# Kernel optimization log

Hardware: AMD Instinct MI355X
Metric: run time of the kernel (lower is better)

## Reference

```python
import jax, jax.numpy as jnp
import numpy as np

NUM_HEADS = 16
WINDOW = 256
DIM = 1024


def setup_inputs() -> dict:
    key = jax.random.key(0)
    k1, k2, k3, k4, k5 = jax.random.split(key, 5)
    B, L, D = 2, 2048, DIM
    s = 1.0 / np.sqrt(D)
    return {
        "x": jax.random.normal(k1, (B, L, D), dtype=jnp.float32),
        "in_proj_w": jax.random.uniform(k2, (3 * D, D), dtype=jnp.float32, minval=-s, maxval=s),
        "in_proj_b": jax.random.uniform(k3, (3 * D,), dtype=jnp.float32, minval=-s, maxval=s),
        "out_w": jax.random.uniform(k4, (D, D), dtype=jnp.float32, minval=-s, maxval=s),
        "out_b": jax.random.uniform(k5, (D,), dtype=jnp.float32, minval=-s, maxval=s),
    }


def reference(x, in_proj_w, in_proj_b, out_w, out_b):
    B, L, D = x.shape
    H = NUM_HEADS
    hd = D // H

    # combined qkv projection, as in nn.MultiheadAttention
    qkv = x @ in_proj_w.T + in_proj_b          # [B, L, 3D]
    q, k, v = jnp.split(qkv, 3, axis=-1)
    q = q.reshape(B, L, H, hd).transpose(0, 2, 1, 3)  # [B, H, L, hd]
    k = k.reshape(B, L, H, hd).transpose(0, 2, 1, 3)
    v = v.reshape(B, L, H, hd).transpose(0, 2, 1, 3)

    scale = 1.0 / jnp.sqrt(jnp.asarray(hd, dtype=x.dtype))
    scores = jnp.einsum("bhqd,bhkd->bhqk", q * scale, k)  # [B, H, L, L]

    # sliding-window causal mask: allowed iff i-window < j <= i
    i = jnp.arange(L)[:, None]
    j = jnp.arange(L)[None, :]
    allowed = (j <= i) & (j > i - WINDOW)                  # [L, L]
    scores = jnp.where(allowed[None, None], scores, -jnp.inf)

    attn = jax.nn.softmax(scores, axis=-1)
    out = jnp.einsum("bhqk,bhkd->bhqd", attn, v)           # [B, H, L, hd]
    out = out.transpose(0, 2, 1, 3).reshape(B, L, D)
    return out @ out_w.T + out_b
```

## Files before the change

kernel.cpp:

```cpp
#include <hip/hip_runtime.h>


#define SEQ_L 2048
#define WIN   256

typedef __bf16 bf16x8 __attribute__((ext_vector_type(8)));
typedef float  f32x4  __attribute__((ext_vector_type(4)));

template<int X> struct ic { static constexpr int v = X; };

__device__ __forceinline__ unsigned short f32_to_bf16(float f) {
  unsigned int u = __float_as_uint(f);
  u += 0x7FFFu + ((u >> 16) & 1u);
  return (unsigned short)(u >> 16);
}

__device__ __forceinline__ void async16(const unsigned short* g, unsigned short* l) {
  __builtin_amdgcn_global_load_lds(
      (const __attribute__((address_space(1))) unsigned int*)g,
      (__attribute__((address_space(3))) unsigned int*)l, 16, 0, 0);
}

__global__ void cast_all(const float* __restrict__ x,  unsigned short* __restrict__ xo,
                         const float* __restrict__ w1, unsigned short* __restrict__ w1o,
                         const float* __restrict__ w2, unsigned short* __restrict__ w2o) {
  int i = blockIdx.x * 256 + threadIdx.x;
  const float* in; unsigned short* out; int k;
  if (i < 1048576)       { in = x;  out = xo;  k = i; }
  else if (i < 1835008)  { in = w1; out = w1o; k = i - 1048576; }
  else                   { in = w2; out = w2o; k = i - 1835008; }
  float4 v = ((const float4*)in)[k];
  ushort4 o;
  o.x = f32_to_bf16(v.x); o.y = f32_to_bf16(v.y);
  o.z = f32_to_bf16(v.z); o.w = f32_to_bf16(v.w);
  ((ushort4*)out)[k] = o;
}

__global__ __launch_bounds__(512, 2) void gemm_qkv(
    const unsigned short* __restrict__ A,
    const unsigned short* __restrict__ Bt,
    const float* __restrict__ bias,
    unsigned short* __restrict__ C, int M, int N, int K)
{
  __shared__ unsigned short As[2][256 * 64];
  __shared__ unsigned short Bs[2][192 * 64];

  const int tid  = threadIdx.x;
  const int lane = tid & 63;
  const int w    = tid >> 6;
  const int wr   = w >> 2;
  const int wc   = w & 3;
  const int quad = lane >> 4;
  const int l16  = lane & 15;
  const int lrow = (lane >> 3) & 7;
  const int scol = (lane & 7) ^ lrow;

  const long m0 = (long)blockIdx.y * 256;
  const long n0 = (long)blockIdx.x * 192;

  f32x4 acc[8][3];
#pragma unroll
  for (int i = 0; i < 8; ++i)
#pragma unroll
    for (int j = 0; j < 3; ++j)
#pragma unroll
      for (int r = 0; r < 4; ++r) acc[i][j][r] = 0.0f;

  auto stA = [&](int buf, int c, int kc) {
    async16(A + (m0 + c * 64 + w * 8 + lrow) * (long)K + kc + scol * 8,
            &As[buf][(c * 64 + w * 8) * 64]);
  };
  auto stB = [&](int buf, int c, int kc) {
    async16(Bt + (n0 + c * 64 + w * 8 + lrow) * (long)K + kc + scol * 8,
            &Bs[buf][(c * 64 + w * 8) * 64]);
  };
  auto hA0 = [&](int buf, int kc) { stA(buf, 0, kc); stA(buf, 2, kc); };
  auto hA1 = [&](int buf, int kc) { stA(buf, 1, kc); stA(buf, 3, kc); };
  auto hB  = [&](int buf, int kc) { stB(buf, 0, kc); stB(buf, 1, kc); stB(buf, 2, kc); };

  auto rdA = [&](bf16x8 (&af)[4], int buf, int QM, int kh) {
#pragma unroll
    for (int mi = 0; mi < 4; ++mi) {
      int rr = wr * 128 + QM * 64 + mi * 16 + l16;
      af[mi] = *(const bf16x8*)&As[buf][rr * 64 + (((kh * 4 + quad) ^ (rr & 7)) << 3)];
    }
  };
  auto rdB = [&](bf16x8 (&bq)[3], int buf, int kh) {
#pragma unroll
    for (int ni = 0; ni < 3; ++ni) {
      int rb = wc * 48 + ni * 16 + l16;
      bq[ni] = *(const bf16x8*)&Bs[buf][rb * 64 + (((kh * 4 + quad) ^ (rb & 7)) << 3)];
    }
  };
  auto cluster = [&](bf16x8 (&af)[4], bf16x8 (&bq)[3], int mb) {
    __builtin_amdgcn_s_setprio(1);
#pragma unroll
    for (int mi = 0; mi < 4; ++mi)
#pragma unroll
      for (int ni = 0; ni < 3; ++ni)
        acc[mb + mi][ni] = __builtin_amdgcn_mfma_f32_16x16x32_bf16(
            bq[ni], af[mi], acc[mb + mi][ni], 0, 0, 0);
    __builtin_amdgcn_s_setprio(0);
  };
  auto lgkm0 = [] {
    asm volatile("s_waitcnt lgkmcnt(0)" ::: "memory");
    __builtin_amdgcn_sched_barrier(0);
  };
  auto vmw = [](auto n) {
    constexpr int V = decltype(n)::v;
    if constexpr (V == 7)      asm volatile("s_waitcnt vmcnt(7)" ::: "memory");
    else if constexpr (V == 2) asm volatile("s_waitcnt vmcnt(2)" ::: "memory");
    else if constexpr (V == 0) asm volatile("s_waitcnt vmcnt(0)" ::: "memory");
  };

  hA0(0, 0); hB(0, 0); hA1(0, 0); hA0(1, 64); hB(1, 64);
  asm volatile("s_waitcnt vmcnt(7)" ::: "memory");
  __builtin_amdgcn_s_barrier();

  auto tile = [&](int T, auto s1, auto s4, auto v1, auto v4) {
    const int buf = T & 1;
    bf16x8 af[4], bq0[3], bq1[3];
    rdA(af, buf, 0, 0);
    rdB(bq0, buf, 0);
    if constexpr (decltype(s1)::v) hA1(buf ^ 1, (T + 1) * 64);
    lgkm0();
    cluster(af, bq0, 0);
    vmw(v1);
    __builtin_amdgcn_s_barrier();
    rdA(af, buf, 1, 0);
    lgkm0();
    cluster(af, bq0, 4);
    rdA(af, buf, 0, 1);
    rdB(bq1, buf, 1);
    lgkm0();
    cluster(af, bq1, 0);
    __builtin_amdgcn_s_barrier();
    rdA(af, buf, 1, 1);
    if constexpr (decltype(s4)::v) { hA0(buf, (T + 2) * 64); hB(buf, (T + 2) * 64); }
    lgkm0();
    cluster(af, bq1, 4);
    vmw(v4);
    __builtin_amdgcn_s_barrier();
  };

  const int NT = K >> 6;
#pragma unroll 1
  for (int T = 0; T < NT - 2; ++T) tile(T, ic<1>{}, ic<1>{}, ic<7>{}, ic<7>{});
  tile(NT - 2, ic<1>{}, ic<0>{}, ic<7>{}, ic<2>{});
  tile(NT - 1, ic<0>{}, ic<0>{}, ic<0>{}, ic<-1>{});

#pragma unroll
  for (int ni = 0; ni < 3; ++ni) {
    const int nb = wc * 48 + ni * 16 + quad * 4;
    const float4 bv = *(const float4*)&bias[n0 + nb];
#pragma unroll
    for (int qm = 0; qm < 2; ++qm)
#pragma unroll
      for (int mi = 0; mi < 4; ++mi) {
        long m = m0 + wr * 128 + qm * 64 + mi * 16 + l16;
        f32x4 a = acc[qm * 4 + mi][ni];
        ushort4 o;
        o.x = f32_to_bf16(a[0] + bv.x);
        o.y = f32_to_bf16(a[1] + bv.y);
        o.z = f32_to_bf16(a[2] + bv.z);
        o.w = f32_to_bf16(a[3] + bv.w);
        *(ushort4*)&C[m * (long)N + n0 + nb] = o;
      }
  }
}

template<int TBM, int TBN, int MI, int NI, int OUTBF>
__global__ __launch_bounds__(256) void gemm_nt(
    const unsigned short* __restrict__ A,
    const unsigned short* __restrict__ Bt,
    const float* __restrict__ bias,
    void* __restrict__ Cout, int M, int N, int K)
{
  __shared__ unsigned short As[TBM * 64];
  __shared__ unsigned short Bs[TBN * 64];

  const int tid  = threadIdx.x;
  const int lane = tid & 63;
  const int wave = tid >> 6;
  const int wr   = (wave >> 1) * (MI * 16);
  const int wc   = (wave & 1) * (NI * 16);
  const int quad = lane >> 4;
  const int l16  = lane & 15;
  const int lrow = lane >> 3;
  const int scol = (lane & 7) ^ lrow;

  const long m0 = (long)blockIdx.y * TBM;
  const long n0 = (long)blockIdx.x * TBN;

  f32x4 acc[MI][NI];
#pragma unroll
  for (int i = 0; i < MI; ++i)
#pragma unroll
    for (int j = 0; j < NI; ++j)
#pragma unroll
      for (int r = 0; r < 4; ++r) acc[i][j][r] = 0.0f;

  for (int k0 = 0; k0 < K; k0 += 64) {
#pragma unroll
    for (int p = 0; p < TBM / 32; ++p) {
      int rb = wave * (TBM / 4) + p * 8;
      async16(A + (m0 + rb + lrow) * (long)K + k0 + scol * 8, &As[rb * 64]);
    }
#pragma unroll
    for (int p = 0; p < TBN / 32; ++p) {
      int rb = wave * (TBN / 4) + p * 8;
      async16(Bt + (n0 + rb + lrow) * (long)K + k0 + scol * 8, &Bs[rb * 64]);
    }
    __syncthreads();
#pragma unroll
    for (int ks = 0; ks < 2; ++ks) {
      bf16x8 af[MI], bfv[NI];
#pragma unroll
      for (int mi = 0; mi < MI; ++mi) {
        int r = wr + mi * 16 + l16;
        af[mi] = *(const bf16x8*)(&As[r * 64 + ((ks * 4 + quad) ^ (r & 7)) * 8]);
      }
#pragma unroll
      for (int ni = 0; ni < NI; ++ni) {
        int r = wc + ni * 16 + l16;
        bfv[ni] = *(const bf16x8*)(&Bs[r * 64 + ((ks * 4 + quad) ^ (r & 7)) * 8]);
      }
#pragma unroll
      for (int mi = 0; mi < MI; ++mi)
#pragma unroll
        for (int ni = 0; ni < NI; ++ni)
          acc[mi][ni] = __builtin_amdgcn_mfma_f32_16x16x32_bf16(af[mi], bfv[ni], acc[mi][ni], 0, 0, 0);
    }
    __syncthreads();
  }

#pragma unroll
  for (int ni = 0; ni < NI; ++ni) {
    long col = n0 + wc + ni * 16 + l16;
    float bv = bias[col];
#pragma unroll
    for (int mi = 0; mi < MI; ++mi) {
      long rowb = m0 + wr + mi * 16 + quad * 4;
#pragma unroll
      for (int r = 0; r < 4; ++r) {
        float v = acc[mi][ni][r] + bv;
        if (OUTBF) ((unsigned short*)Cout)[(rowb + r) * N + col] = f32_to_bf16(v);
        else       ((float*)Cout)[(rowb + r) * N + col] = v;
      }
    }
  }
}

__global__ __launch_bounds__(256) void attn_kernel(
    const unsigned short* __restrict__ qkv,
    unsigned short* __restrict__ aout)
{
  __shared__ unsigned short Ks[64 * 72];
  __shared__ unsigned short Vt[64 * 72];
  __shared__ unsigned short Ps[4 * 16 * 72];

  const int tid  = threadIdx.x;
  const int w    = tid >> 6;
  const int lane = tid & 63;
  const int quad = lane >> 4;
  const int l16  = lane & 15;

  const int blk = blockIdx.x;
  const int qb  = blk & 15;
  const int h   = (blk >> 4) & 15;
  const int b   = blk >> 8;

  const int  i0 = qb * 128;
  const long rowbase = (long)b * SEQ_L;

  bf16x8 aq[2][2];
#pragma unroll
  for (int sub = 0; sub < 2; ++sub) {
    const unsigned short* qp =
        qkv + (rowbase + i0 + sub * 64 + w * 16 + l16) * 3072 + h * 64 + quad * 8;
    aq[sub][0] = *(const bf16x8*)(qp);
    aq[sub][1] = *(const bf16x8*)(qp + 32);
  }

  f32x4 o[2][4];
  float l_i[2][4];
#pragma unroll
  for (int sub = 0; sub < 2; ++sub)
#pragma unroll
    for (int ni = 0; ni < 4; ++ni)
#pragma unroll
      for (int r = 0; r < 4; ++r) { o[sub][ni][r] = 0.0f; l_i[sub][r] = 0.0f; }

  unsigned short* psw = &Ps[w * 16 * 72];

  const int j_begin = (i0 >= WIN) ? i0 - WIN : 0;

  for (int j0 = j_begin; j0 < i0 + 128; j0 += 64) {
    __syncthreads();
#pragma unroll
    for (int p = 0; p < 2; ++p) {
      int c = p * 256 + tid, row = c >> 3, col8 = c & 7;
      const unsigned short* base = qkv + (rowbase + j0 + row) * 3072 + h * 64 + col8 * 8;
      *(uint4*)(&Ks[row * 72 + col8 * 8]) = *(const uint4*)(base + 1024);
      unsigned short tmp[8];
      *(uint4*)tmp = *(const uint4*)(base + 2048);
      int rsw = row ^ (col8 << 3);
#pragma unroll
      for (int e = 0; e < 8; ++e)
        Vt[(col8 * 8 + e) * 72 + rsw] = tmp[e];
    }
    __syncthreads();

    bf16x8 kf[4][2];
#pragma unroll
    for (int g = 0; g < 4; ++g) {
      kf[g][0] = *(const bf16x8*)(&Ks[(g * 16 + l16) * 72 + quad * 8]);
      kf[g][1] = *(const bf16x8*)(&Ks[(g * 16 + l16) * 72 + 32 + quad * 8]);
    }
    bf16x8 vf[2][4];
#pragma unroll
    for (int kk = 0; kk < 2; ++kk)
#pragma unroll
      for (int ni = 0; ni < 4; ++ni) {
        int d  = ni * 16 + l16;
        int rb = (kk * 32 + quad * 8) ^ (((d >> 3) & 7) << 3);
        vf[kk][ni] = *(const bf16x8*)(&Vt[d * 72 + rb]);
      }

#pragma unroll
    for (int sub = 0; sub < 2; ++sub) {
      const int i0s = i0 + sub * 64 + w * 16;
      if (j0 > i0s + 15) continue;
      if (j0 + 63 + WIN <= i0s) continue;

      f32x4 s[4];
#pragma unroll
      for (int g = 0; g < 4; ++g) {
        f32x4 z;
#pragma unroll
        for (int r = 0; r < 4; ++r) z[r] = 0.0f;
        z = __builtin_amdgcn_mfma_f32_16x16x32_bf16(aq[sub][0], kf[g][0], z, 0, 0, 0);
        z = __builtin_amdgcn_mfma_f32_16x16x32_bf16(aq[sub][1], kf[g][1], z, 0, 0, 0);
        s[g] = z;
      }
#pragma unroll
      for (int g = 0; g < 4; ++g) {
        int j = j0 + g * 16 + l16;
#pragma unroll
        for (int r = 0; r < 4; ++r) {
          int i = i0s + quad * 4 + r;
          bool ok = (j <= i) && (j > i - WIN);
          float e = ok ? __expf(s[g][r] * 0.125f) : 0.0f;
          psw[(quad * 4 + r) * 72 + g * 16 + l16] = f32_to_bf16(e);
          l_i[sub][r] += e;
        }
      }
      asm volatile("s_waitcnt lgkmcnt(0)" ::: "memory");
#pragma unroll
      for (int kk = 0; kk < 2; ++kk) {
        bf16x8 ap = *(const bf16x8*)(&psw[l16 * 72 + kk * 32 + quad * 8]);
#pragma unroll
        for (int ni = 0; ni < 4; ++ni)
          o[sub][ni] = __builtin_amdgcn_mfma_f32_16x16x32_bf16(ap, vf[kk][ni], o[sub][ni], 0, 0, 0);
      }
    }
  }

#pragma unroll
  for (int sub = 0; sub < 2; ++sub)
#pragma unroll
    for (int r = 0; r < 4; ++r) {
      float rs = l_i[sub][r];
      rs += __shfl_xor(rs, 1);
      rs += __shfl_xor(rs, 2);
      rs += __shfl_xor(rs, 4);
      rs += __shfl_xor(rs, 8);
      float inv_l = 1.0f / rs;
      long row = rowbase + i0 + sub * 64 + w * 16 + quad * 4 + r;
#pragma unroll
      for (int ni = 0; ni < 4; ++ni)
        aout[row * 1024 + h * 64 + ni * 16 + l16] = f32_to_bf16(o[sub][ni][r] * inv_l);
    }
}

extern "C" void kernel_launch(void* const* d_in, const int* in_sizes, int n_in,
                              void* d_out, int out_size, void* d_ws, size_t ws_size,
                              hipStream_t stream)
{
  const float* x  = (const float*)d_in[0];
  const float* w1 = (const float*)d_in[1];
  const float* b1 = (const float*)d_in[2];
  const float* w2 = (const float*)d_in[3];
  const float* b2 = (const float*)d_in[4];
  float* out = (float*)d_out;

  char* ws = (char*)d_ws;
  unsigned short* x_bf   = (unsigned short*)(ws);
  unsigned short* w1_bf  = (unsigned short*)(ws + 8388608);
  unsigned short* w2_bf  = (unsigned short*)(ws + 14680064);
  unsigned short* qkv_bf = (unsigned short*)(ws + 16777216);
  unsigned short* at_bf  = (unsigned short*)(ws + 41943040);

  cast_all<<<8192, 256, 0, stream>>>(x, x_bf, w1, w1_bf, w2, w2_bf);

  dim3 g1(3072 / 192, 4096 / 256);
  gemm_qkv<<<g1, 512, 0, stream>>>(x_bf, w1_bf, b1, qkv_bf, 4096, 3072, 1024);

  attn_kernel<<<512, 256, 0, stream>>>(qkv_bf, at_bf);

  dim3 g2(1024 / 64, 4096 / 64);
  gemm_nt<64, 64, 2, 2, 0><<<g2, 256, 0, stream>>>(at_bf, w2_bf, b2, out, 4096, 1024, 1024);
}
```

Measured before the change: 155.0 us.

## Replace output projection GEMM with double-buffered 128x128 pipelined kernel

```diff
diff --git a/kernel.cpp b/kernel.cpp
--- a/kernel.cpp
+++ b/kernel.cpp
@@ -169,84 +169,120 @@
   }
 }
 
-template<int TBM, int TBN, int MI, int NI, int OUTBF>
-__global__ __launch_bounds__(256) void gemm_nt(
+__global__ __launch_bounds__(512, 4) void gemm_opj(
     const unsigned short* __restrict__ A,
     const unsigned short* __restrict__ Bt,
     const float* __restrict__ bias,
-    void* __restrict__ Cout, int M, int N, int K)
+    float* __restrict__ C, int M, int N, int K)
 {
-  __shared__ unsigned short As[TBM * 64];
-  __shared__ unsigned short Bs[TBN * 64];
+  __shared__ unsigned short As[2][128 * 64];
+  __shared__ unsigned short Bs[2][128 * 64];
 
   const int tid  = threadIdx.x;
   const int lane = tid & 63;
-  const int wave = tid >> 6;
-  const int wr   = (wave >> 1) * (MI * 16);
-  const int wc   = (wave & 1) * (NI * 16);
+  const int w    = tid >> 6;
+  const int wr   = w >> 2;
+  const int wc   = w & 3;
   const int quad = lane >> 4;
   const int l16  = lane & 15;
-  const int lrow = lane >> 3;
+  const int lrow = (lane >> 3) & 7;
   const int scol = (lane & 7) ^ lrow;
 
-  const long m0 = (long)blockIdx.y * TBM;
-  const long n0 = (long)blockIdx.x * TBN;
-
-  f32x4 acc[MI][NI];
-#pragma unroll
-  for (int i = 0; i < MI; ++i)
-#pragma unroll
-    for (int j = 0; j < NI; ++j)
+  const long m0 = (long)blockIdx.y * 128;
+  const long n0 = (long)blockIdx.x * 128;
+
+  f32x4 acc[4][2];
+#pragma unroll
+  for (int i = 0; i < 4; ++i)
+#pragma unroll
+    for (int j = 0; j < 2; ++j)
 #pragma unroll
       for (int r = 0; r < 4; ++r) acc[i][j][r] = 0.0f;
 
-  for (int k0 = 0; k0 < K; k0 += 64) {
-#pragma unroll
-    for (int p = 0; p < TBM / 32; ++p) {
-      int rb = wave * (TBM / 4) + p * 8;
-      async16(A + (m0 + rb + lrow) * (long)K + k0 + scol * 8, &As[rb * 64]);
-    }
-#pragma unroll
-    for (int p = 0; p < TBN / 32; ++p) {
-      int rb = wave * (TBN / 4) + p * 8;
-      async16(Bt + (n0 + rb + lrow) * (long)K + k0 + scol * 8, &Bs[rb * 64]);
-    }
-    __syncthreads();
-#pragma unroll
-    for (int ks = 0; ks < 2; ++ks) {
-      bf16x8 af[MI], bfv[NI];
-#pragma unroll
-      for (int mi = 0; mi < MI; ++mi) {
-        int r = wr + mi * 16 + l16;
-        af[mi] = *(const bf16x8*)(&As[r * 64 + ((ks * 4 + quad) ^ (r & 7)) * 8]);
-      }
-#pragma unroll
-      for (int ni = 0; ni < NI; ++ni) {
-        int r = wc + ni * 16 + l16;
-        bfv[ni] = *(const bf16x8*)(&Bs[r * 64 + ((ks * 4 + quad) ^ (r & 7)) * 8]);
-      }
-#pragma unroll
-      for (int mi = 0; mi < MI; ++mi)
-#pragma unroll
-        for (int ni = 0; ni < NI; ++ni)
-          acc[mi][ni] = __builtin_amdgcn_mfma_f32_16x16x32_bf16(af[mi], bfv[ni], acc[mi][ni], 0, 0, 0);
-    }
-    __syncthreads();
-  }
-
-#pragma unroll
-  for (int ni = 0; ni < NI; ++ni) {
-    long col = n0 + wc + ni * 16 + l16;
-    float bv = bias[col];
-#pragma unroll
-    for (int mi = 0; mi < MI; ++mi) {
-      long rowb = m0 + wr + mi * 16 + quad * 4;
-#pragma unroll
-      for (int r = 0; r < 4; ++r) {
-        float v = acc[mi][ni][r] + bv;
-        if (OUTBF) ((unsigned short*)Cout)[(rowb + r) * N + col] = f32_to_bf16(v);
-        else       ((float*)Cout)[(rowb + r) * N + col] = v;
-      }
+  auto stage = [&](int buf, int kc) {
+#pragma unroll
+    for (int c = 0; c < 2; ++c)
+      async16(A + (m0 + c * 64 + w * 8 + lrow) * (long)K + kc + scol * 8,
+              &As[buf][(c * 64 + w * 8) * 64]);
+#pragma unroll
+    for (int c = 0; c < 2; ++c)
+      async16(Bt + (n0 + c * 64 + w * 8 + lrow) * (long)K + kc + scol * 8,
+              &Bs[buf][(c * 64 + w * 8) * 64]);
+  };
+
+  auto rdA = [&](bf16x8 (&af)[4], int buf, int kh) {
+#pragma unroll
+    for (int mi = 0; mi < 4; ++mi) {
+      int rr = wr * 64 + mi * 16 + l16;
+      af[mi] = *(const bf16x8*)&As[buf][rr * 64 + (((kh * 4 + quad) ^ (rr & 7)) << 3)];
+    }
+  };
+  auto rdB = [&](bf16x8 (&bq)[2], int buf, int kh) {
+#pragma unroll
+    for (int ni = 0; ni < 2; ++ni) {
+      int rb = wc * 32 + ni * 16 + l16;
+      bq[ni] = *(const bf16x8*)&Bs[buf][rb * 64 + (((kh * 4 + quad) ^ (rb & 7)) << 3)];
+    }
+  };
+  auto cluster = [&](bf16x8 (&af)[4], bf16x8 (&bq)[2]) {
+    __builtin_amdgcn_s_setprio(1);
+#pragma unroll
+    for (int mi = 0; mi < 4; ++mi)
+#pragma unroll
+      for (int ni = 0; ni < 2; ++ni)
+        acc[mi][ni] = __builtin_amdgcn_mfma_f32_16x16x32_bf16(
+            bq[ni], af[mi], acc[mi][ni], 0, 0, 0);
+    __builtin_amdgcn_s_setprio(0);
+  };
+  auto lgkm0 = [] {
+    asm volatile("s_waitcnt lgkmcnt(0)" ::: "memory");
+    __builtin_amdgcn_sched_barrier(0);
+  };
+
+  stage(0, 0); stage(1, 64);
+  asm volatile("s_waitcnt vmcnt(4)" ::: "memory");
+  __builtin_amdgcn_s_barrier();
+
+  auto tile = [&](int T, auto s, auto v) {
+    const int buf = T & 1;
+    bf16x8 af[4], bq[2];
+    rdA(af, buf, 0);
+    rdB(bq, buf, 0);
+    lgkm0();
+    cluster(af, bq);
+    rdA(af, buf, 1);
+    rdB(bq, buf, 1);
+    lgkm0();
+    __builtin_amdgcn_s_barrier();
+    if constexpr (decltype(s)::v) stage(buf, (T + 2) * 64);
+    cluster(af, bq);
+    if constexpr (decltype(v)::v == 4)
+      asm volatile("s_waitcnt vmcnt(4)" ::: "memory");
+    else if constexpr (decltype(v)::v == 0)
+      asm volatile("s_waitcnt vmcnt(0)" ::: "memory");
+    __builtin_amdgcn_s_barrier();
+  };
+
+  const int NT = K >> 6;
+#pragma unroll 1
+  for (int T = 0; T < NT - 2; ++T) tile(T, ic<1>{}, ic<4>{});
+  tile(NT - 2, ic<0>{}, ic<0>{});
+  tile(NT - 1, ic<0>{}, ic<-1>{});
+
+#pragma unroll
+  for (int ni = 0; ni < 2; ++ni) {
+    const int nb = wc * 32 + ni * 16 + quad * 4;
+    const float4 bv = *(const float4*)&bias[n0 + nb];
+#pragma unroll
+    for (int mi = 0; mi < 4; ++mi) {
+      long m = m0 + wr * 64 + mi * 16 + l16;
+      f32x4 a = acc[mi][ni];
+      float4 o;
+      o.x = a[0] + bv.x;
+      o.y = a[1] + bv.y;
+      o.z = a[2] + bv.z;
+      o.w = a[3] + bv.w;
+      *(float4*)&C[m * (long)N + n0 + nb] = o;
     }
   }
 }
@@ -408,6 +444,6 @@
 
   attn_kernel<<<512, 256, 0, stream>>>(qkv_bf, at_bf);
 
-  dim3 g2(1024 / 64, 4096 / 64);
-  gemm_nt<64, 64, 2, 2, 0><<<g2, 256, 0, stream>>>(at_bf, w2_bf, b2, out, 4096, 1024, 1024);
-}
+  dim3 g2(1024 / 128, 4096 / 128);
+  gemm_opj<<<g2, 512, 0, stream>>>(at_bf, w2_bf, b2, out, 4096, 1024, 1024);
+}
```

Result: no change. 156.7 us (+1.1%).

## Prefetch all LDS fragments per tile and use partial lgkmcnt waits

Applied to the files above, without the earlier changes.

```diff
diff --git a/kernel.cpp b/kernel.cpp
--- a/kernel.cpp
+++ b/kernel.cpp
@@ -102,8 +102,11 @@
             bq[ni], af[mi], acc[mb + mi][ni], 0, 0, 0);
     __builtin_amdgcn_s_setprio(0);
   };
-  auto lgkm0 = [] {
-    asm volatile("s_waitcnt lgkmcnt(0)" ::: "memory");
+  auto lgkm = [](auto n) {
+    constexpr int V = decltype(n)::v;
+    if constexpr (V == 8)      asm volatile("s_waitcnt lgkmcnt(8)" ::: "memory");
+    else if constexpr (V == 4) asm volatile("s_waitcnt lgkmcnt(4)" ::: "memory");
+    else                       asm volatile("s_waitcnt lgkmcnt(0)" ::: "memory");
     __builtin_amdgcn_sched_barrier(0);
   };
   auto vmw = [](auto n) {
@@ -117,29 +120,28 @@
   asm volatile("s_waitcnt vmcnt(7)" ::: "memory");
   __builtin_amdgcn_s_barrier();
 
-  auto tile = [&](int T, auto s1, auto s4, auto v1, auto v4) {
+  auto tile = [&](int T, auto s1, auto s4, auto vS, auto vE) {
     const int buf = T & 1;
-    bf16x8 af[4], bq0[3], bq1[3];
-    rdA(af, buf, 0, 0);
-    rdB(bq0, buf, 0);
+    bf16x8 af00[4], af10[4], af01[4], af11[4], bq0[3], bq1[3];
+    rdA(af00, buf, 0, 0);
+    rdB(bq0,  buf, 0);
+    rdA(af01, buf, 0, 1);
+    rdB(bq1,  buf, 1);
     if constexpr (decltype(s1)::v) hA1(buf ^ 1, (T + 1) * 64);
-    lgkm0();
-    cluster(af, bq0, 0);
-    vmw(v1);
+    vmw(vS);
     __builtin_amdgcn_s_barrier();
-    rdA(af, buf, 1, 0);
-    lgkm0();
-    cluster(af, bq0, 4);
-    rdA(af, buf, 0, 1);
-    rdB(bq1, buf, 1);
-    lgkm0();
-    cluster(af, bq1, 0);
+    rdA(af10, buf, 1, 0);
+    rdA(af11, buf, 1, 1);
+    lgkm(ic<8>{});
+    cluster(af00, bq0, 0);
+    lgkm(ic<4>{});
+    cluster(af10, bq0, 4);
+    cluster(af01, bq1, 0);
+    lgkm(ic<0>{});
     __builtin_amdgcn_s_barrier();
-    rdA(af, buf, 1, 1);
     if constexpr (decltype(s4)::v) { hA0(buf, (T + 2) * 64); hB(buf, (T + 2) * 64); }
-    lgkm0();
-    cluster(af, bq1, 4);
-    vmw(v4);
+    cluster(af11, bq1, 4);
+    if constexpr (decltype(vE)::v >= 0) vmw(vE);
     __builtin_amdgcn_s_barrier();
   };
 
```

New measurement: 157.5 us. No clear change (+1.6%).

## Fuse activation fp32-to-bf16 cast into QKV GEMM A-tile loading

Applied to the files above, without the earlier changes.

```diff
diff --git a/kernel.cpp b/kernel.cpp
--- a/kernel.cpp
+++ b/kernel.cpp
@@ -21,14 +21,12 @@
       (__attribute__((address_space(3))) unsigned int*)l, 16, 0, 0);
 }
 
-__global__ void cast_all(const float* __restrict__ x,  unsigned short* __restrict__ xo,
-                         const float* __restrict__ w1, unsigned short* __restrict__ w1o,
-                         const float* __restrict__ w2, unsigned short* __restrict__ w2o) {
+__global__ void cast_w(const float* __restrict__ w1, unsigned short* __restrict__ w1o,
+                       const float* __restrict__ w2, unsigned short* __restrict__ w2o) {
   int i = blockIdx.x * 256 + threadIdx.x;
   const float* in; unsigned short* out; int k;
-  if (i < 1048576)       { in = x;  out = xo;  k = i; }
-  else if (i < 1835008)  { in = w1; out = w1o; k = i - 1048576; }
-  else                   { in = w2; out = w2o; k = i - 1835008; }
+  if (i < 786432) { in = w1; out = w1o; k = i; }
+  else            { in = w2; out = w2o; k = i - 786432; }
   float4 v = ((const float4*)in)[k];
   ushort4 o;
   o.x = f32_to_bf16(v.x); o.y = f32_to_bf16(v.y);
@@ -37,7 +35,7 @@
 }
 
 __global__ __launch_bounds__(512, 2) void gemm_qkv(
-    const unsigned short* __restrict__ A,
+    const float* __restrict__ X,
     const unsigned short* __restrict__ Bt,
     const float* __restrict__ bias,
     unsigned short* __restrict__ C, int M, int N, int K)
@@ -53,7 +51,8 @@
   const int quad = lane >> 4;
   const int l16  = lane & 15;
   const int lrow = (lane >> 3) & 7;
-  const int scol = (lane & 7) ^ lrow;
+  const int lcol = lane & 7;
+  const int scol = lcol ^ lrow;
 
   const long m0 = (long)blockIdx.y * 256;
   const long n0 = (long)blockIdx.x * 192;
@@ -66,17 +65,32 @@
 #pragma unroll
       for (int r = 0; r < 4; ++r) acc[i][j][r] = 0.0f;
 
-  auto stA = [&](int buf, int c, int kc) {
-    async16(A + (m0 + c * 64 + w * 8 + lrow) * (long)K + kc + scol * 8,
-            &As[buf][(c * 64 + w * 8) * 64]);
-  };
+  float4 rA[8];
+  auto loadA = [&](int kc) {
+#pragma unroll
+    for (int c = 0; c < 4; ++c) {
+      const float* src = X + (m0 + c * 64 + w * 8 + lrow) * (long)K + kc + lcol * 8;
+      rA[c * 2]     = *(const float4*)(src);
+      rA[c * 2 + 1] = *(const float4*)(src + 4);
+    }
+  };
+  auto writeA = [&](int buf) {
+#pragma unroll
+    for (int c = 0; c < 4; ++c) {
+      unsigned short tmp[8];
+      tmp[0] = f32_to_bf16(rA[c * 2].x);     tmp[1] = f32_to_bf16(rA[c * 2].y);
+      tmp[2] = f32_to_bf16(rA[c * 2].z);     tmp[3] = f32_to_bf16(rA[c * 2].w);
+      tmp[4] = f32_to_bf16(rA[c * 2 + 1].x); tmp[5] = f32_to_bf16(rA[c * 2 + 1].y);
+      tmp[6] = f32_to_bf16(rA[c * 2 + 1].z); tmp[7] = f32_to_bf16(rA[c * 2 + 1].w);
+      *(uint4*)&As[buf][(c * 64 + w * 8 + lrow) * 64 + (lcol ^ lrow) * 8] = *(uint4*)tmp;
+    }
+  };
+
   auto stB = [&](int buf, int c, int kc) {
     async16(Bt + (n0 + c * 64 + w * 8 + lrow) * (long)K + kc + scol * 8,
             &Bs[buf][(c * 64 + w * 8) * 64]);
   };
-  auto hA0 = [&](int buf, int kc) { stA(buf, 0, kc); stA(buf, 2, kc); };
-  auto hA1 = [&](int buf, int kc) { stA(buf, 1, kc); stA(buf, 3, kc); };
-  auto hB  = [&](int buf, int kc) { stB(buf, 0, kc); stB(buf, 1, kc); stB(buf, 2, kc); };
+  auto hB = [&](int buf, int kc) { stB(buf, 0, kc); stB(buf, 1, kc); stB(buf, 2, kc); };
 
   auto rdA = [&](bf16x8 (&af)[4], int buf, int QM, int kh) {
 #pragma unroll
@@ -106,48 +120,47 @@
     asm volatile("s_waitcnt lgkmcnt(0)" ::: "memory");
     __builtin_amdgcn_sched_barrier(0);
   };
-  auto vmw = [](auto n) {
-    constexpr int V = decltype(n)::v;
-    if constexpr (V == 7)      asm volatile("s_waitcnt vmcnt(7)" ::: "memory");
-    else if constexpr (V == 2) asm volatile("s_waitcnt vmcnt(2)" ::: "memory");
-    else if constexpr (V == 0) asm volatile("s_waitcnt vmcnt(0)" ::: "memory");
-  };
-
-  hA0(0, 0); hB(0, 0); hA1(0, 0); hA0(1, 64); hB(1, 64);
-  asm volatile("s_waitcnt vmcnt(7)" ::: "memory");
+
+  hB(0, 0);
+  loadA(0);
+  hB(1, 64);
+  asm volatile("s_waitcnt vmcnt(3)" ::: "memory");
+  writeA(0);
+  lgkm0();
   __builtin_amdgcn_s_barrier();
 
-  auto tile = [&](int T, auto s1, auto s4, auto v1, auto v4) {
+  auto tile = [&](int T, auto sA, auto sB) {
     const int buf = T & 1;
     bf16x8 af[4], bq0[3], bq1[3];
     rdA(af, buf, 0, 0);
     rdB(bq0, buf, 0);
-    if constexpr (decltype(s1)::v) hA1(buf ^ 1, (T + 1) * 64);
+    if constexpr (decltype(sA)::v) loadA((T + 1) * 64);
     lgkm0();
     cluster(af, bq0, 0);
-    vmw(v1);
-    __builtin_amdgcn_s_barrier();
     rdA(af, buf, 1, 0);
     lgkm0();
-    cluster(af, bq0, 4);
+    cluster(af, bq0, 2 * 2);
     rdA(af, buf, 0, 1);
     rdB(bq1, buf, 1);
     lgkm0();
     cluster(af, bq1, 0);
     __builtin_amdgcn_s_barrier();
     rdA(af, buf, 1, 1);
-    if constexpr (decltype(s4)::v) { hA0(buf, (T + 2) * 64); hB(buf, (T + 2) * 64); }
+    if constexpr (decltype(sA)::v) {
+      asm volatile("s_waitcnt vmcnt(0)" ::: "memory");
+      writeA(buf ^ 1);
+    }
+    if constexpr (decltype(sB)::v) hB(buf, (T + 2) * 64);
     lgkm0();
     cluster(af, bq1, 4);
-    vmw(v4);
     __builtin_amdgcn_s_barrier();
   };
 
   const int NT = K >> 6;
 #pragma unroll 1
-  for (int T = 0; T < NT - 2; ++T) tile(T, ic<1>{}, ic<1>{}, ic<7>{}, ic<7>{});
-  tile(NT - 2, ic<1>{}, ic<0>{}, ic<7>{}, ic<2>{});
-  tile(NT - 1, ic<0>{}, ic<0>{}, ic<0>{}, ic<-1>{});
+  for (int T = 0; T < NT - 2; ++T) tile(T, ic<1>{}, ic<1>{});
+  tile(NT - 2, ic<1>{}, ic<0>{});
+  tile(NT - 1, ic<0>{}, ic<0>{});
 
 #pragma unroll
   for (int ni = 0; ni < 3; ++ni) {
@@ -395,16 +408,15 @@
   float* out = (float*)d_out;
 
   char* ws = (char*)d_ws;
-  unsigned short* x_bf   = (unsigned short*)(ws);
   unsigned short* w1_bf  = (unsigned short*)(ws + 8388608);
   unsigned short* w2_bf  = (unsigned short*)(ws + 14680064);
   unsigned short* qkv_bf = (unsigned short*)(ws + 16777216);
   unsigned short* at_bf  = (unsigned short*)(ws + 41943040);
 
-  cast_all<<<8192, 256, 0, stream>>>(x, x_bf, w1, w1_bf, w2, w2_bf);
+  cast_w<<<4096, 256, 0, stream>>>(w1, w1_bf, w2, w2_bf);
 
   dim3 g1(3072 / 192, 4096 / 256);
-  gemm_qkv<<<g1, 512, 0, stream>>>(x_bf, w1_bf, b1, qkv_bf, 4096, 3072, 1024);
+  gemm_qkv<<<g1, 512, 0, stream>>>(x, w1_bf, b1, qkv_bf, 4096, 3072, 1024);
 
   attn_kernel<<<512, 256, 0, stream>>>(qkv_bf, at_bf);
 
```

Result: slower. 167.1 us (+7.8%).
